# Kernel optimization log

Hardware: AMD Instinct MI355X
Metric: run time of the kernel (lower is better)

## Reference

```python
import jax, jax.numpy as jnp
import numpy as np
from jax.scipy.special import betaln

V, E, H, Z = 50000, 300, 200, 30  # vocab, emb, enc hidden, z_rnn_size
B, T = 64, 512
L, R = -0.1, 1.1  # HardKuma stretched support


def setup_inputs() -> dict:
    key = jax.random.key(0)
    ks = jax.random.split(key, 16)
    s = 0.05  # weight scale to keep gates in a sane range
    return {
        "x": jax.random.randint(ks[0], (B, T), 0, V),
        "mask": jnp.ones((B, T), dtype=bool),
        "emb_W": jax.random.normal(ks[1], (V, E), jnp.float32) * 0.1,
        "enc_Wi_f": jax.random.normal(ks[2], (E, 4 * H), jnp.float32) * s,
        "enc_Wh_f": jax.random.normal(ks[3], (H, 4 * H), jnp.float32) * s,
        "enc_b_f": jnp.zeros((4 * H,), jnp.float32),
        "enc_Wi_b": jax.random.normal(ks[4], (E, 4 * H), jnp.float32) * s,
        "enc_Wh_b": jax.random.normal(ks[5], (H, 4 * H), jnp.float32) * s,
        "enc_b_b": jnp.zeros((4 * H,), jnp.float32),
        "z_Wi": jax.random.normal(ks[6], (2 * H + 1, 4 * Z), jnp.float32) * s,
        "z_Wh": jax.random.normal(ks[7], (Z, 4 * Z), jnp.float32) * s,
        "z_b": jnp.zeros((4 * Z,), jnp.float32),
        "kuma_Wa": jax.random.normal(ks[8], (2 * H + Z, 1), jnp.float32) * s,
        "kuma_ba": jnp.zeros((1,), jnp.float32),
        "kuma_Wb": jax.random.normal(ks[9], (2 * H + Z, 1), jnp.float32) * s,
        "kuma_bb": jnp.zeros((1,), jnp.float32),
    }


def _lstm_scan(xt, Wi, Wh, b, reverse):
    # xt: [T, B, E] -> outputs h: [T, B, H]; torch gate order i, f, g, o
    Bsz = xt.shape[1]
    Hd = Wh.shape[0]
    x_proj = xt @ Wi + b  # precompute input projection [T, B, 4H]

    def step(carry, xp):
        h, c = carry
        g = xp + h @ Wh
        i, f, gg, o = jnp.split(g, 4, axis=-1)
        c = jax.nn.sigmoid(f) * c + jax.nn.sigmoid(i) * jnp.tanh(gg)
        h = jax.nn.sigmoid(o) * jnp.tanh(c)
        return (h, c), h

    init = (jnp.zeros((Bsz, Hd), xt.dtype), jnp.zeros((Bsz, Hd), xt.dtype))
    _, hs = jax.lax.scan(step, init, x_proj, reverse=reverse)
    return hs


def reference(x, mask, emb_W, enc_Wi_f, enc_Wh_f, enc_b_f, enc_Wi_b, enc_Wh_b,
              enc_b_b, z_Wi, z_Wh, z_b, kuma_Wa, kuma_ba, kuma_Wb, kuma_bb):
    # eval-mode forward (dropout = identity, deterministic HardKuma branch)
    emb = emb_W[x]                       # [B, T, E]
    xt = emb.transpose(1, 0, 2)          # [T, B, E]
    hf = _lstm_scan(xt, enc_Wi_f, enc_Wh_f, enc_b_f, False)
    hb = _lstm_scan(xt, enc_Wi_b, enc_Wh_b, enc_b_b, True)
    h = jnp.concatenate([hf, hb], axis=-1)  # [T, B, 2H]

    x0 = (0.0 - L) / (R - L)
    x1 = (1.0 - L) / (R - L)

    def step(carry, h_t):
        zh, zc = carry                    # LSTMCell state, each [B, Z]
        gin = jnp.concatenate([h_t, zh], axis=-1)  # [B, 2H+Z]
        a = jnp.clip(jax.nn.softplus(gin @ kuma_Wa + kuma_ba), 1e-6, 100.0)
        b = jnp.clip(jax.nn.softplus(gin @ kuma_Wb + kuma_bb), 1e-6, 100.0)
        # HardKuma point masses: p0 = F(x0), p1 = 1 - F(x1); F(x)=1-(1-x^a)^b
        p0 = 1.0 - (1.0 - x0 ** a) ** b
        p1 = (1.0 - x1 ** a) ** b
        pc = 1.0 - p0 - p1
        kmean = jnp.exp(betaln(1.0 + 1.0 / a, b) + jnp.log(b))  # Kuma mean
        smean = L + (R - L) * kmean       # stretched mean
        zero_one = jnp.where(p0 > p1, 0.0, 1.0)
        z_t = jnp.where((pc > p0) & (pc > p1), smean, zero_one)  # [B, 1]
        rnn_in = jnp.concatenate([h_t, z_t], axis=-1)  # [B, 2H+1]
        g = rnn_in @ z_Wi + zh @ z_Wh + z_b
        i, f, gg, o = jnp.split(g, 4, axis=-1)
        zc = jax.nn.sigmoid(f) * zc + jax.nn.sigmoid(i) * jnp.tanh(gg)
        zh = jax.nn.sigmoid(o) * jnp.tanh(zc)
        return (zh, zc), z_t[:, 0]

    Bsz = h.shape[1]
    init = (jnp.zeros((Bsz, Z), h.dtype), jnp.zeros((Bsz, Z), h.dtype))
    _, zs = jax.lax.scan(step, init, h)   # zs: [T, B]
    z = zs.T                              # [B, T]
    return jnp.where(mask, z, 0.0)
```

## Files before the change

kernel.cpp:

```cpp
#include <hip/hip_runtime.h>


#define T_LEN 512
#define NBATCH 64
#define EMB 300
#define HID 200

typedef __attribute__((ext_vector_type(2))) _Float16 half2v;
typedef __attribute__((ext_vector_type(8))) _Float16 f16x8;
typedef __attribute__((ext_vector_type(4))) float f32x4;

union HU16 { _Float16 h; unsigned short u; };
union U32H2 { unsigned int u; half2v h; };

__device__ __forceinline__ half2v h2_from_u32(unsigned int u) { U32H2 v; v.u = u; return v.h; }
__device__ __forceinline__ unsigned int u32_from_h2(half2v h) { U32H2 v; v.h = h; return v.u; }
__device__ __forceinline__ half2v h2_pack(float a, float b) {
  half2v h; h.x = (_Float16)a; h.y = (_Float16)b; return h;
}
__device__ __forceinline__ float fdot2f(half2v a, half2v b, float c) {
#if __has_builtin(__builtin_amdgcn_fdot2)
  return __builtin_amdgcn_fdot2(a, b, c, false);
#else
  return (float)a.x * (float)b.x + (float)a.y * (float)b.y + c;
#endif
}
__device__ __forceinline__ float sigmf(float x) { return 1.0f / (1.0f + __expf(-x)); }
__device__ __forceinline__ float tanhfast(float x) {
  float ax = fabsf(x);
  float t = __expf(-2.0f * ax);
  float r = (1.0f - t) / (1.0f + t);
  return x < 0.0f ? -r : r;
}
__device__ __forceinline__ float softplus_fast(float x) {
  return fmaxf(x, 0.0f) + __logf(1.0f + __expf(-fabsf(x)));
}
__device__ __forceinline__ float lgamma_pos6(float z) {
  const float w = z + 6.0f;
  const float prod = (z * (z + 1.f)) * ((z + 2.f) * (z + 3.f)) * ((z + 4.f) * (z + 5.f));
  const float iw = 1.0f / w;
  const float iw2 = iw * iw;
  const float ser = iw * (0.0833333333f + iw2 * (-0.00277777778f + iw2 * 0.000793650794f));
  return (w - 0.5f) * __logf(w) - w + 0.91893853320467f + ser - __logf(prod);
}
__device__ __forceinline__ float hardkuma_z(float apre, float bpre) {
  const float a = fminf(fmaxf(softplus_fast(apre), 1e-6f), 100.0f);
  const float b = fminf(fmaxf(softplus_fast(bpre), 1e-6f), 100.0f);
  const float lx0 = -2.48490664979f;
  const float lx1 = -0.08701137698f;
  const float u0 = __expf(a * lx0) - 1.0f;
  const float p0 = 1.0f - __expf(b * __logf(-u0));
  const float u1 = __expf(a * lx1) - 1.0f;
  const float p1 = __expf(b * __logf(-u1));
  const float pc = 1.0f - p0 - p1;
  const float ia = 1.0f / a;
  const float lbeta = lgamma_pos6(1.0f + ia) + lgamma_pos6(b) - lgamma_pos6(1.0f + ia + b);
  const float kmean = __expf(lbeta + __logf(b));
  const float smean = -0.1f + 1.2f * kmean;
  const float zo = (p0 > p1) ? 0.0f : 1.0f;
  return (pc > p0 && pc > p1) ? smean : zo;
}

__global__ __launch_bounds__(256) void wit_kernel(
    const float* __restrict__ WiF, const float* __restrict__ WiB, _Float16* __restrict__ WiT)
{
  const int o = blockIdx.x * 256 + threadIdx.x;
  const int dir = o / (896 * 320);
  const int rem = o - dir * 896 * 320;
  const int n = rem / 320;
  const int k = rem - n * 320;
  const float* Wi = dir ? WiB : WiF;
  float v = (n < 800 && k < EMB) ? Wi[(size_t)k * 800 + n] : 0.0f;
  WiT[o] = (_Float16)v;
}

__global__ __launch_bounds__(320) void abuf_kernel(
    const int* __restrict__ xids, const float* __restrict__ embW, _Float16* __restrict__ Abuf)
{
  const int r = blockIdx.x;
  const int t = r >> 6;
  const int b = r & 63;
  const int k = threadIdx.x;
  const size_t row = (size_t)xids[b * T_LEN + t];
  float v = (k < EMB) ? embW[row * EMB + k] : 0.0f;
  Abuf[(size_t)r * 320 + k] = (_Float16)v;
}

__global__ __launch_bounds__(256) void proj_kernel(
    const _Float16* __restrict__ Abuf, const _Float16* __restrict__ WiT,
    const float* __restrict__ biasF, const float* __restrict__ biasB,
    _Float16* __restrict__ xp)
{
  const int t = blockIdx.x;
  const int nbase = blockIdx.y * 128;
  const int dir = blockIdx.z;
  const float* bias = dir ? biasB : biasF;

  const int tid = threadIdx.x;
  const int w = tid >> 6;
  const int lane = tid & 63;
  const int m16 = lane & 15;
  const int q = lane >> 4;

  f32x4 acc[8];
#pragma unroll
  for (int i = 0; i < 8; ++i) acc[i] = (f32x4){0.f, 0.f, 0.f, 0.f};

  const _Float16* arow = Abuf + ((size_t)t * 64 + w * 16 + m16) * 320;
  const _Float16* bbase = WiT + ((size_t)dir * 896) * 320;

  for (int kt = 0; kt < 10; ++kt) {
    const int kk = kt * 32 + q * 8;
    const f16x8 af = *(const f16x8*)(arow + kk);
#pragma unroll
    for (int nt = 0; nt < 8; ++nt) {
      const f16x8 bf = *(const f16x8*)(bbase + (size_t)(nbase + nt * 16 + m16) * 320 + kk);
      acc[nt] = __builtin_amdgcn_mfma_f32_16x16x32_f16(af, bf, acc[nt], 0, 0, 0);
    }
  }
#pragma unroll
  for (int nt = 0; nt < 8; ++nt) {
    const int cg = nbase + nt * 16 + m16;
    if (cg < 800) {
      const float bv = bias[cg];
#pragma unroll
      for (int reg = 0; reg < 4; ++reg) {
        const int brow = w * 16 + q * 4 + reg;
        xp[((size_t)(dir * 64 + brow) * T_LEN + t) * 800 + cg] = (_Float16)(acc[nt][reg] + bv);
      }
    }
  }
}

__global__ __launch_bounds__(1024) void lstm_kernel(
    const float* __restrict__ WhF, const float* __restrict__ WhB,
    const _Float16* __restrict__ xp, _Float16* __restrict__ hout)
{
  const int chain = blockIdx.x;
  const int b = chain & 63;
  const int dir = chain >> 6;
  const float* Wh = dir ? WhB : WhF;
  const int tid = threadIdx.x;
  const int q = tid >> 8;
  const int m = tid & 255;
  const bool active = m < HID;

  __shared__ __align__(16) unsigned int shm[20000];

  unsigned int wq[4][25];
  for (int k = 0; k < 4; ++k) {
    __syncthreads();
    for (int j = tid; j < 40000; j += 1024) {
      const int rl = j / 800;
      const int col = j - rl * 800;
      HU16 hu; hu.h = (_Float16)Wh[(size_t)(50 * k + rl) * 800 + col];
      ((unsigned short*)shm)[col * 50 + rl] = hu.u;
    }
    __syncthreads();
    if (active && q == k) {
#pragma unroll
      for (int g = 0; g < 4; ++g) {
        const int base = (g * 200 + m) * 25;
#pragma unroll
        for (int p = 0; p < 25; ++p) wq[g][p] = shm[base + p];
      }
    }
  }
  __syncthreads();
  for (int j = tid; j < 20000; j += 1024) shm[j] = 0u;
  __syncthreads();
  float* part = (float*)(shm + 256);

  float cst = 0.0f;
  const bool cellt = active && (q == 0);
  const _Float16* xprow = xp + (size_t)(dir * 64 + b) * T_LEN * 800;
  float xc[4] = {0.f, 0.f, 0.f, 0.f};
  if (cellt) {
    const _Float16* xpt = xprow + (size_t)(dir ? (T_LEN - 1) : 0) * 800 + m;
#pragma unroll
    for (int g = 0; g < 4; ++g) xc[g] = (float)xpt[g * 200];
  }

  for (int s = 0; s < T_LEN; ++s) {
    const int t = dir ? (T_LEN - 1 - s) : s;
    if (active) {
      const unsigned int* hq = shm + (s & 1) * 128 + q * 25;
      float a0 = 0.f, a1 = 0.f, a2 = 0.f, a3 = 0.f;
#pragma unroll
      for (int p = 0; p < 25; ++p) {
        const half2v hp = h2_from_u32(hq[p]);
        a0 = fdot2f(hp, h2_from_u32(wq[0][p]), a0);
        a1 = fdot2f(hp, h2_from_u32(wq[1][p]), a1);
        a2 = fdot2f(hp, h2_from_u32(wq[2][p]), a2);
        a3 = fdot2f(hp, h2_from_u32(wq[3][p]), a3);
      }
      part[(0 * 4 + q) * 256 + m] = a0;
      part[(1 * 4 + q) * 256 + m] = a1;
      part[(2 * 4 + q) * 256 + m] = a2;
      part[(3 * 4 + q) * 256 + m] = a3;
    }
    __syncthreads();
    if (cellt) {
      float pre[4];
#pragma unroll
      for (int g = 0; g < 4; ++g) {
        pre[g] = part[(g * 4 + 0) * 256 + m] + part[(g * 4 + 1) * 256 + m]
               + part[(g * 4 + 2) * 256 + m] + part[(g * 4 + 3) * 256 + m] + xc[g];
      }
      const float gi = sigmf(pre[0]);
      const float gf = sigmf(pre[1]);
      const float gg = tanhfast(pre[2]);
      const float go = sigmf(pre[3]);
      cst = gf * cst + gi * gg;
      const float hm = go * tanhfast(cst);
      HU16 hu; hu.h = (_Float16)hm;
      ((unsigned short*)shm)[((s + 1) & 1) * 256 + m] = hu.u;
      hout[((size_t)t * 64 + b) * 400 + dir * HID + m] = hu.h;
      if ((s + 1) < T_LEN) {
        const int tn = dir ? (t - 1) : (t + 1);
        const _Float16* xpt = xprow + (size_t)tn * 800 + m;
#pragma unroll
        for (int g = 0; g < 4; ++g) xc[g] = (float)xpt[g * 200];
      }
    }
    __syncthreads();
  }
}

__global__ __launch_bounds__(256) void bt_kernel(
    const float* __restrict__ kWa, const float* __restrict__ kWb,
    const float* __restrict__ zWi, _Float16* __restrict__ BT)
{
  const int o = blockIdx.x * 256 + threadIdx.x;
  const int n = o / 416;
  const int k = o - n * 416;
  float v = 0.0f;
  if (k < 400) {
    if (n == 0) v = kWa[k];
    else if (n == 1) v = kWb[k];
    else if (n < 122) v = zWi[(size_t)k * 120 + (n - 2)];
  }
  BT[o] = (_Float16)v;
}

__global__ __launch_bounds__(256, 1) void pre_gemm(
    const _Float16* __restrict__ hout, const _Float16* __restrict__ BT,
    float* __restrict__ pre)
{
  const int bid = blockIdx.x;
  const int tid = threadIdx.x;
  const int w = tid >> 6;
  const int lane = tid & 63;
  const int m16 = lane & 15;
  const int q = lane >> 4;

  f32x4 acc[8];
#pragma unroll
  for (int i = 0; i < 8; ++i) acc[i] = (f32x4){0.f, 0.f, 0.f, 0.f};

  const _Float16* arow = hout + ((size_t)bid * 64 + w * 16 + m16) * 400;
#pragma unroll
  for (int kf = 0; kf < 13; ++kf) {
    const int kk = kf * 32 + q * 8;
    const int ka = (kk < 400) ? kk : 0;
    const f16x8 af = *(const f16x8*)(arow + ka);
#pragma unroll
    for (int nt = 0; nt < 8; ++nt) {
      const f16x8 bf = *(const f16x8*)(BT + (size_t)(nt * 16 + m16) * 416 + kk);
      acc[nt] = __builtin_amdgcn_mfma_f32_16x16x32_f16(af, bf, acc[nt], 0, 0, 0);
    }
  }
#pragma unroll
  for (int nt = 0; nt < 8; ++nt) {
    const int col = nt * 16 + m16;
#pragma unroll
    for (int reg = 0; reg < 4; ++reg) {
      const int row = w * 16 + q * 4 + reg;
      pre[((size_t)bid * 64 + row) * 128 + col] = acc[nt][reg];
    }
  }
}

__global__ __attribute__((amdgpu_flat_work_group_size(64, 64), amdgpu_waves_per_eu(1, 1)))
void zscan_kernel(
    const float* __restrict__ pre,
    const float* __restrict__ zWi, const float* __restrict__ zWh, const float* __restrict__ zb,
    const float* __restrict__ kWa, const float* __restrict__ kba,
    const float* __restrict__ kWb, const float* __restrict__ kbb,
    float* __restrict__ out)
{
  const int b = blockIdx.x;
  const int l = threadIdx.x;
  const bool cell = l < 30;

  half2v wg[4][15];
  float zb4[4] = {0.f, 0.f, 0.f, 0.f}, wz4[4] = {0.f, 0.f, 0.f, 0.f};
#pragma unroll
  for (int j = 0; j < 4; ++j) {
    const int col = cell ? (l + 30 * j) : 0;
#pragma unroll
    for (int p = 0; p < 15; ++p) {
      const float wa = zWh[(size_t)(2 * p) * 120 + col];
      const float wb = zWh[(size_t)(2 * p + 1) * 120 + col];
      wg[j][p] = cell ? h2_pack(wa, wb) : h2_pack(0.f, 0.f);
    }
    if (cell) { zb4[j] = zb[col]; wz4[j] = zWi[(size_t)400 * 120 + col]; }
  }
  half2v kwa[15], kwb[15];
#pragma unroll
  for (int p = 0; p < 15; ++p) {
    kwa[p] = h2_pack(kWa[400 + 2 * p], kWa[400 + 2 * p + 1]);
    kwb[p] = h2_pack(kWb[400 + 2 * p], kWb[400 + 2 * p + 1]);
  }
  const float kbaS = kba[0], kbbS = kbb[0];

  float zc = 0.f, zhf = 0.f;

  const float* prow = pre + (size_t)b * 128;
  float pv[4];
  float pk0, pk1;
  {
    const int lc = cell ? l : 0;
#pragma unroll
    for (int j = 0; j < 4; ++j) pv[j] = prow[2 + lc + 30 * j];
    pk0 = prow[0]; pk1 = prow[1];
  }

  for (int t = 0; t < T_LEN; ++t) {
    float cur[4];
#pragma unroll
    for (int j = 0; j < 4; ++j) cur[j] = cell ? pv[j] : 0.f;
    const float ck0 = pk0, ck1 = pk1;
    if ((t + 1) < T_LEN) {
      const float* prn = prow + (size_t)(t + 1) * 64 * 128;
      const int lc = cell ? l : 0;
#pragma unroll
      for (int j = 0; j < 4; ++j) pv[j] = prn[2 + lc + 30 * j];
      pk0 = prn[0]; pk1 = prn[1];
    }
    const float zn = __shfl_xor(zhf, 1);
    const unsigned int zp = u32_from_h2(h2_pack(zhf, zn));
    half2v zhp[15];
#pragma unroll
    for (int p = 0; p < 15; ++p)
      zhp[p] = h2_from_u32((unsigned int)__shfl((int)zp, 2 * p));
    float aa = ck0 + kbaS, ab = 0.f, ba = ck1 + kbbS, bb = 0.f;
#pragma unroll
    for (int p = 0; p < 15; p += 2) {
      aa = fdot2f(zhp[p], kwa[p], aa);
      ba = fdot2f(zhp[p], kwb[p], ba);
      if (p + 1 < 15) {
        ab = fdot2f(zhp[p + 1], kwa[p + 1], ab);
        bb = fdot2f(zhp[p + 1], kwb[p + 1], bb);
      }
    }
    const float zt = hardkuma_z(aa + ab, ba + bb);
    if (l == 0) out[(size_t)b * T_LEN + t] = zt;

    float gq[4];
#pragma unroll
    for (int j = 0; j < 4; ++j) {
      float s0 = cur[j] + zb4[j], s1 = 0.f;
#pragma unroll
      for (int p = 0; p < 15; p += 2) {
        s0 = fdot2f(zhp[p], wg[j][p], s0);
        if (p + 1 < 15) s1 = fdot2f(zhp[p + 1], wg[j][p + 1], s1);
      }
      gq[j] = s0 + s1 + wz4[j] * zt;
    }
    zc = sigmf(gq[1]) * zc + sigmf(gq[0]) * tanhfast(gq[2]);
    zhf = sigmf(gq[3]) * tanhfast(zc);
  }
}

extern "C" void kernel_launch(void* const* d_in, const int* in_sizes, int n_in,
                              void* d_out, int out_size, void* d_ws, size_t ws_size,
                              hipStream_t stream)
{
  const int*   x    = (const int*)d_in[0];
  const float* embW = (const float*)d_in[2];
  const float* WiF  = (const float*)d_in[3];
  const float* WhF  = (const float*)d_in[4];
  const float* bF   = (const float*)d_in[5];
  const float* WiB  = (const float*)d_in[6];
  const float* WhB  = (const float*)d_in[7];
  const float* bB   = (const float*)d_in[8];
  const float* zWi  = (const float*)d_in[9];
  const float* zWh  = (const float*)d_in[10];
  const float* zb   = (const float*)d_in[11];
  const float* kWa  = (const float*)d_in[12];
  const float* kba  = (const float*)d_in[13];
  const float* kWb  = (const float*)d_in[14];
  const float* kbb  = (const float*)d_in[15];
  float* out = (float*)d_out;

  char* ws = (char*)d_ws;
  _Float16* xp   = (_Float16*)ws;
  _Float16* WiT  = (_Float16*)(ws + 104857600);
  _Float16* Abuf = (_Float16*)(ws + 106004480);
  _Float16* hout = (_Float16*)(ws + 104857600);
  _Float16* BT   = (_Float16*)ws;
  float*    pre  = (float*)(ws + 33554432);

  wit_kernel <<<dim3(2240), 256, 0, stream>>>(WiF, WiB, WiT);
  abuf_kernel<<<dim3(32768), 320, 0, stream>>>(x, embW, Abuf);
  proj_kernel<<<dim3(T_LEN, 7, 2), 256, 0, stream>>>(Abuf, WiT, bF, bB, xp);
  lstm_kernel<<<dim3(128), 1024, 0, stream>>>(WhF, WhB, xp, hout);
  bt_kernel  <<<dim3(208), 256, 0, stream>>>(kWa, kWb, zWi, BT);
  pre_gemm   <<<dim3(T_LEN), 256, 0, stream>>>(hout, BT, pre);
  zscan_kernel<<<dim3(NBATCH), 64, 0, stream>>>(pre, zWi, zWh, zb, kWa, kba, kWb, kbb, out);
}
```

Before: 1.760 ms.

## Reduce LSTM gate partial sums with DPP within quads, dropping a barrier

The recurrent step now maps the four k-slices of each hidden unit to adjacent lanes instead of separate 256-thread groups. Partial dot products are combined with DPP quad swizzles rather than being written to shared memory and summed by a single thread group after a barrier. This removes one __syncthreads and the shared-memory partial buffer per time step, and lets every lane compute the gate nonlinearities redundantly. The hidden state is stored with a padded stride of 28 words so it can be read as 16-byte vectors. The risk is the redundant transcendental work across all four lanes, plus the changed hidden-state indexing.

Result: slower. 1.892 ms (+7.5%).

```diff
diff --git a/kernel.cpp b/kernel.cpp
--- a/kernel.cpp
+++ b/kernel.cpp
@@ -9,6 +9,7 @@
 typedef __attribute__((ext_vector_type(2))) _Float16 half2v;
 typedef __attribute__((ext_vector_type(8))) _Float16 f16x8;
 typedef __attribute__((ext_vector_type(4))) float f32x4;
+typedef __attribute__((ext_vector_type(4))) unsigned int u32x4;
 
 union HU16 { _Float16 h; unsigned short u; };
 union U32H2 { unsigned int u; half2v h; };
@@ -24,6 +25,11 @@
 #else
   return (float)a.x * (float)b.x + (float)a.y * (float)b.y + c;
 #endif
+}
+template <int CTRL>
+__device__ __forceinline__ float qp_add(float x) {
+  const int y = __builtin_amdgcn_update_dpp(0, __float_as_int(x), CTRL, 0xF, 0xF, true);
+  return x + __int_as_float(y);
 }
 __device__ __forceinline__ float sigmf(float x) { return 1.0f / (1.0f + __expf(-x)); }
 __device__ __forceinline__ float tanhfast(float x) {
@@ -141,9 +147,10 @@
   const int dir = chain >> 6;
   const float* Wh = dir ? WhB : WhF;
   const int tid = threadIdx.x;
-  const int q = tid >> 8;
-  const int m = tid & 255;
+  const int m = tid >> 2;
+  const int q = tid & 3;
   const bool active = m < HID;
+  const bool lead = active && (q == 0);
 
   __shared__ __align__(16) unsigned int shm[20000];
 
@@ -169,58 +176,71 @@
   __syncthreads();
   for (int j = tid; j < 20000; j += 1024) shm[j] = 0u;
   __syncthreads();
-  float* part = (float*)(shm + 256);
+
+  const int hw_u16 = (m / 50) * 56 + (m % 50);
 
   float cst = 0.0f;
-  const bool cellt = active && (q == 0);
   const _Float16* xprow = xp + (size_t)(dir * 64 + b) * T_LEN * 800;
-  float xc[4] = {0.f, 0.f, 0.f, 0.f};
-  if (cellt) {
+  float xc0 = 0.f, xc1 = 0.f, xc2 = 0.f, xc3 = 0.f;
+  if (lead) {
     const _Float16* xpt = xprow + (size_t)(dir ? (T_LEN - 1) : 0) * 800 + m;
-#pragma unroll
-    for (int g = 0; g < 4; ++g) xc[g] = (float)xpt[g * 200];
+    xc0 = (float)xpt[0];
+    xc1 = (float)xpt[200];
+    xc2 = (float)xpt[400];
+    xc3 = (float)xpt[600];
   }
 
   for (int s = 0; s < T_LEN; ++s) {
     const int t = dir ? (T_LEN - 1 - s) : s;
     if (active) {
-      const unsigned int* hq = shm + (s & 1) * 128 + q * 25;
-      float a0 = 0.f, a1 = 0.f, a2 = 0.f, a3 = 0.f;
-#pragma unroll
-      for (int p = 0; p < 25; ++p) {
-        const half2v hp = h2_from_u32(hq[p]);
-        a0 = fdot2f(hp, h2_from_u32(wq[0][p]), a0);
-        a1 = fdot2f(hp, h2_from_u32(wq[1][p]), a1);
-        a2 = fdot2f(hp, h2_from_u32(wq[2][p]), a2);
-        a3 = fdot2f(hp, h2_from_u32(wq[3][p]), a3);
-      }
-      part[(0 * 4 + q) * 256 + m] = a0;
-      part[(1 * 4 + q) * 256 + m] = a1;
-      part[(2 * 4 + q) * 256 + m] = a2;
-      part[(3 * 4 + q) * 256 + m] = a3;
-    }
-    __syncthreads();
-    if (cellt) {
-      float pre[4];
-#pragma unroll
-      for (int g = 0; g < 4; ++g) {
-        pre[g] = part[(g * 4 + 0) * 256 + m] + part[(g * 4 + 1) * 256 + m]
-               + part[(g * 4 + 2) * 256 + m] + part[(g * 4 + 3) * 256 + m] + xc[g];
-      }
-      const float gi = sigmf(pre[0]);
-      const float gf = sigmf(pre[1]);
-      const float gg = tanhfast(pre[2]);
-      const float go = sigmf(pre[3]);
+      float a0 = (q == 0) ? xc0 : 0.0f;
+      float a1 = (q == 0) ? xc1 : 0.0f;
+      float a2 = (q == 0) ? xc2 : 0.0f;
+      float a3 = (q == 0) ? xc3 : 0.0f;
+      const unsigned int* hqw = shm + (s & 1) * 128 + q * 28;
+      const u32x4* hq4 = (const u32x4*)hqw;
+#pragma unroll
+      for (int c = 0; c < 6; ++c) {
+        const u32x4 hv = hq4[c];
+#pragma unroll
+        for (int e = 0; e < 4; ++e) {
+          const half2v hp = h2_from_u32(hv[e]);
+          const int p = c * 4 + e;
+          a0 = fdot2f(hp, h2_from_u32(wq[0][p]), a0);
+          a1 = fdot2f(hp, h2_from_u32(wq[1][p]), a1);
+          a2 = fdot2f(hp, h2_from_u32(wq[2][p]), a2);
+          a3 = fdot2f(hp, h2_from_u32(wq[3][p]), a3);
+        }
+      }
+      {
+        const half2v hp = h2_from_u32(hqw[24]);
+        a0 = fdot2f(hp, h2_from_u32(wq[0][24]), a0);
+        a1 = fdot2f(hp, h2_from_u32(wq[1][24]), a1);
+        a2 = fdot2f(hp, h2_from_u32(wq[2][24]), a2);
+        a3 = fdot2f(hp, h2_from_u32(wq[3][24]), a3);
+      }
+      a0 = qp_add<0xB1>(a0); a0 = qp_add<0x4E>(a0);
+      a1 = qp_add<0xB1>(a1); a1 = qp_add<0x4E>(a1);
+      a2 = qp_add<0xB1>(a2); a2 = qp_add<0x4E>(a2);
+      a3 = qp_add<0xB1>(a3); a3 = qp_add<0x4E>(a3);
+      const float gi = sigmf(a0);
+      const float gf = sigmf(a1);
+      const float gg = tanhfast(a2);
+      const float go = sigmf(a3);
       cst = gf * cst + gi * gg;
       const float hm = go * tanhfast(cst);
-      HU16 hu; hu.h = (_Float16)hm;
-      ((unsigned short*)shm)[((s + 1) & 1) * 256 + m] = hu.u;
-      hout[((size_t)t * 64 + b) * 400 + dir * HID + m] = hu.h;
-      if ((s + 1) < T_LEN) {
-        const int tn = dir ? (t - 1) : (t + 1);
-        const _Float16* xpt = xprow + (size_t)tn * 800 + m;
-#pragma unroll
-        for (int g = 0; g < 4; ++g) xc[g] = (float)xpt[g * 200];
+      if (q == 0) {
+        HU16 hu; hu.h = (_Float16)hm;
+        ((unsigned short*)shm)[((s + 1) & 1) * 256 + hw_u16] = hu.u;
+        hout[((size_t)t * 64 + b) * 400 + dir * HID + m] = hu.h;
+        if ((s + 1) < T_LEN) {
+          const int tn = dir ? (t - 1) : (t + 1);
+          const _Float16* xpt = xprow + (size_t)tn * 800 + m;
+          xc0 = (float)xpt[0];
+          xc1 = (float)xpt[200];
+          xc2 = (float)xpt[400];
+          xc3 = (float)xpt[600];
+        }
       }
     }
     __syncthreads();
```
